# Performance work log

Hardware: AMD Instinct MI355X
Metric: run time of the kernel (lower is better)

## Reference

```python
import jax, jax.numpy as jnp
import numpy as np
from jax import lax

D_MODEL = 1024
D_INNER = 2048
B = 8
T = 2048
INIT_ALPHA_BIAS = 2.0


def setup_inputs() -> dict:
    key = jax.random.key(0)
    ks = jax.random.split(key, 6)
    def xavier(k, shape):
        fan_in, fan_out = shape[1], shape[0]
        lim = float(np.sqrt(6.0 / (fan_in + fan_out)))
        return jax.random.uniform(k, shape, jnp.float32, -lim, lim)
    return {
        "x": jax.random.normal(ks[0], (B, T, D_MODEL), jnp.float32),
        "h0": jnp.zeros((B, D_INNER), jnp.float32),
        "W_in": xavier(ks[1], (D_INNER, D_MODEL)),
        "W_alpha": xavier(ks[2], (D_INNER, D_INNER)),
        "b_alpha": jnp.full((D_INNER,), INIT_ALPHA_BIAS, jnp.float32),
        "W_v": xavier(ks[3], (D_INNER, D_INNER)),
        "b_v": jnp.zeros((D_INNER,), jnp.float32),
        "W_out": xavier(ks[4], (D_MODEL, D_INNER)),
    }


def reference(x, h0, W_in, W_alpha, b_alpha, W_v, b_v, W_out):
    # in_proj + silu pre-activation: [B,T,D_inner]
    x_proj = jax.nn.silu(jnp.einsum('btd,id->bti', x, W_in))
    # time-major for the scan: [T,B,D_inner]
    xr = jnp.transpose(x_proj, (1, 0, 2))
    # precompute gate and value for all steps (big GEMMs)
    alpha = jax.nn.sigmoid(jnp.einsum('tbd,ed->tbe', xr, W_alpha) + b_alpha)
    v = jnp.einsum('tbd,ed->tbe', xr, W_v) + b_v

    def step(h, av):
        a, vt = av
        h_new = a * h + (1.0 - a) * vt  # decay-gated update
        out_t = h_new * jax.nn.silu(h_new)  # self-gating
        return h_new, out_t

    h_final, outs = lax.scan(step, h0, (alpha, v))  # outs: [T,B,D_inner]
    # out_proj back to model dim, batch-major: [B,T,D_model]
    output = jnp.einsum('tbe,de->btd', outs, W_out)
    return output, h_final
```

## Files before the change

kernel.cpp:

```cpp
#include <hip/hip_runtime.h>
#include <cstdint>
#include <cstddef>

typedef unsigned short u16;
typedef unsigned int   u32;

#define D_MODEL 1024
#define D_INNER 2048
#define BATCH   8
#define TSEQ    2048
#define MROWS   (BATCH*TSEQ)
#define CHUNK   32
#define NCHUNK  (TSEQ/CHUNK)
#define EDIM    (BATCH*D_INNER)

typedef float  f32x4  __attribute__((ext_vector_type(4)));
typedef __bf16 bf16x8 __attribute__((ext_vector_type(8)));
typedef short  s16x8  __attribute__((ext_vector_type(8)));

__device__ __forceinline__ float bf2f(u16 u){ return __builtin_bit_cast(float, (u32)u << 16); }
__device__ __forceinline__ u16 f2bf(float f){
  u32 u = __builtin_bit_cast(u32, f);
  u += 0x7fffu + ((u >> 16) & 1u);
  return (u16)(u >> 16);
}
__device__ __forceinline__ float sigm(float x){ return 1.0f/(1.0f + __expf(-x)); }

__device__ __forceinline__ void gld16(const u16* g, u16* l){
  __builtin_amdgcn_global_load_lds((const __attribute__((address_space(1))) void*)g,
                                   (__attribute__((address_space(3))) void*)l, 16, 0, 0);
}

__device__ __forceinline__ s16x8 cvt8(const float* s){
  float4 u0 = *(const float4*)s;
  float4 u1 = *(const float4*)(s + 4);
  s16x8 p;
  p[0]=(short)f2bf(u0.x); p[1]=(short)f2bf(u0.y);
  p[2]=(short)f2bf(u0.z); p[3]=(short)f2bf(u0.w);
  p[4]=(short)f2bf(u1.x); p[5]=(short)f2bf(u1.y);
  p[6]=(short)f2bf(u1.z); p[7]=(short)f2bf(u1.w);
  return p;
}

template<int MODE, int K, int N>
__global__ __launch_bounds__(512, 2) void gemm256(
    const u16* __restrict__ A, const u16* __restrict__ Bt,
    const float* __restrict__ bias, const float* __restrict__ bias2,
    void* __restrict__ Cout, void* __restrict__ Cout2)
{
  __shared__ __align__(16) u16 sAB[2][2][16384];
  constexpr int NT = K/64;
  const int tid = threadIdx.x;
  const int w = tid >> 6, lane = tid & 63;
  const int wr = w >> 2, wc = w & 3;
  const int l15 = lane & 15, kg = lane >> 4;
  const int bm = blockIdx.x, bn = blockIdx.y;

  const int st_rw   = lane >> 3;
  const int st_cole = ((lane&7) ^ st_rw) << 3;
  const size_t a_base = (size_t)(bm*256)*K + st_cole;
  const size_t b_base = (size_t)(bn*256)*K + st_cole;

  auto stageA = [&](int buf, int kt, int set){
    u16* dst = &sAB[0][buf][set*4096 + w*512];
    #pragma unroll
    for (int i = 0; i < 2; ++i){
      const int row = set*64 + i*128 + w*8 + st_rw;
      gld16(A + a_base + (size_t)row*K + kt*64, dst + i*8192);
    }
  };
  auto stageB = [&](int buf, int kt, int set){
    #pragma unroll
    for (int i = 0; i < 2; ++i){
      const int g = i*64 + w*8;
      const int rowbase = (g>>5)*64 + set*32 + (g&31);
      gld16(Bt + b_base + (size_t)(rowbase + st_rw)*K + kt*64,
            &sAB[1][buf][rowbase*64]);
    }
  };

  const int csw = (kg*16) ^ ((l15&7)<<4);

  f32x4 acc[8][4] = {};

  stageB(0,0,0); stageB(0,0,1); stageA(0,0,0); stageA(0,0,1);

  for (int t = 0; t < NT; ++t){
    const char* As = (const char*)&sAB[0][t&1][0];
    const char* Bs = (const char*)&sAB[1][t&1][0];
    const int nb = (t+1)&1;

    asm volatile("s_waitcnt vmcnt(0)" ::: "memory");
    __builtin_amdgcn_s_barrier();

    if (t < NT-1){
      stageB(nb,t+1,0); stageB(nb,t+1,1); stageA(nb,t+1,0); stageA(nb,t+1,1);
    }

    s16x8 bf[4][2];
    #pragma unroll
    for (int ni = 0; ni < 4; ++ni){
      bf[ni][0] = *(const s16x8*)(Bs + (wc*64 + ni*16 + l15)*128 + csw);
      bf[ni][1] = *(const s16x8*)(Bs + (wc*64 + ni*16 + l15)*128 + (csw^64));
    }
    #pragma unroll
    for (int mh = 0; mh < 2; ++mh){
      s16x8 af[4][2];
      #pragma unroll
      for (int mf = 0; mf < 4; ++mf){
        af[mf][0] = *(const s16x8*)(As + (wr*128 + mh*64 + mf*16 + l15)*128 + csw);
        af[mf][1] = *(const s16x8*)(As + (wr*128 + mh*64 + mf*16 + l15)*128 + (csw^64));
      }
      #pragma unroll
      for (int mf = 0; mf < 4; ++mf)
        #pragma unroll
        for (int ni = 0; ni < 4; ++ni)
          #pragma unroll
          for (int ks = 0; ks < 2; ++ks)
            acc[mh*4+mf][ni] = __builtin_amdgcn_mfma_f32_16x16x32_bf16(
                __builtin_bit_cast(bf16x8, af[mf][ks]),
                __builtin_bit_cast(bf16x8, bf[ni][ks]),
                acc[mh*4+mf][ni], 0, 0, 0);
    }
  }

  #pragma unroll
  for (int mi = 0; mi < 8; ++mi){
    #pragma unroll
    for (int ni = 0; ni < 4; ++ni){
      #pragma unroll
      for (int r = 0; r < 4; ++r){
        const int row = bm*256 + wr*128 + mi*16 + kg*4 + r;
        const int col = bn*256 + wc*64 + ni*16 + l15;
        float val = acc[mi][ni][r];
        if constexpr (MODE == 0){
          val = val * sigm(val);
          ((u16*)Cout)[(size_t)row*N + col] = f2bf(val);
        } else if constexpr (MODE == 3){
          const int orow = (row & 7)*TSEQ + (row >> 3);
          ((float*)Cout)[(size_t)orow*N + col] = val;
        } else if constexpr (MODE == 4){
          if (col < D_INNER){
            val = sigm(val + bias[col]);
            ((u16*)Cout)[(size_t)row*D_INNER + col] = f2bf(val);
          } else {
            val = val + bias2[col - D_INNER];
            ((u16*)Cout2)[(size_t)row*D_INNER + (col - D_INNER)] = f2bf(val);
          }
        }
      }
    }
  }
}

template<int MODE, int K, int N, bool BA, bool BB>
__global__ __launch_bounds__(256) void gemm_bt(
    const void* __restrict__ Ap, const void* __restrict__ Bp,
    const float* __restrict__ bias, void* __restrict__ Cout)
{
  __shared__ __align__(16) u16 sA[128*32];
  __shared__ __align__(16) u16 sB[128*32];
  const int tid = threadIdx.x;
  const int bm = blockIdx.x, bn = blockIdx.y;
  const int w = tid >> 6, lane = tid & 63;
  const int wr = w >> 1, wc = w & 1;
  const int l15 = lane & 15, kg = lane >> 4;
  const int r0   = tid >> 2;
  const int koff = (tid & 3) * 8;

  int ga[2];
  #pragma unroll
  for (int i = 0; i < 2; ++i){
    int mc = bm*128 + r0 + i*64;
    if (MODE == 0)      ga[i] = (mc & 7) * TSEQ + (mc >> 3);
    else if (MODE == 3) ga[i] = (mc & (TSEQ-1)) * BATCH + (mc >> 11);
    else                ga[i] = mc;
  }
  const u16*   Abf = (const u16*)Ap;
  const float* Af  = (const float*)Ap;
  const u16*   Bbf = (const u16*)Bp;
  const float* Bf  = (const float*)Bp;
  u16* la[2] = { sA + w*512, sA + 2048 + w*512 };
  u16* lb[2] = { sB + w*512, sB + 2048 + w*512 };
  u16* ldsA = sA + tid*8;
  u16* ldsB = sB + tid*8;
  const int gb[2] = { bn*128 + r0, bn*128 + r0 + 64 };

  f32x4 acc[4][4] = {};
  for (int kt = 0; kt < K/32; ++kt){
    __syncthreads();
    if constexpr (BA){
      gld16(Abf + (size_t)ga[0]*K + koff + kt*32, la[0]);
      gld16(Abf + (size_t)ga[1]*K + koff + kt*32, la[1]);
    } else {
      #pragma unroll
      for (int i = 0; i < 2; ++i)
        *(s16x8*)(ldsA + i*2048) = cvt8(Af + (size_t)ga[i]*K + koff + kt*32);
    }
    if constexpr (BB){
      gld16(Bbf + (size_t)gb[0]*K + koff + kt*32, lb[0]);
      gld16(Bbf + (size_t)gb[1]*K + koff + kt*32, lb[1]);
    } else {
      #pragma unroll
      for (int i = 0; i < 2; ++i)
        *(s16x8*)(ldsB + i*2048) = cvt8(Bf + (size_t)gb[i]*K + koff + kt*32);
    }
    __syncthreads();

    s16x8 af[4], bfr[4];
    #pragma unroll
    for (int m = 0; m < 4; ++m)
      af[m] = *(const s16x8*)(sA + (wr*64 + m*16 + l15)*32 + kg*8);
    #pragma unroll
    for (int n = 0; n < 4; ++n)
      bfr[n] = *(const s16x8*)(sB + (wc*64 + n*16 + l15)*32 + kg*8);
    #pragma unroll
    for (int m = 0; m < 4; ++m)
      #pragma unroll
      for (int n = 0; n < 4; ++n)
        acc[m][n] = __builtin_amdgcn_mfma_f32_16x16x32_bf16(
            __builtin_bit_cast(bf16x8, af[m]),
            __builtin_bit_cast(bf16x8, bfr[n]),
            acc[m][n], 0, 0, 0);
  }
  #pragma unroll
  for (int m = 0; m < 4; ++m)
    #pragma unroll
    for (int n = 0; n < 4; ++n)
      #pragma unroll
      for (int r = 0; r < 4; ++r){
        const int row = bm*128 + wr*64 + m*16 + kg*4 + r;
        const int col = bn*128 + wc*64 + n*16 + l15;
        float val = acc[m][n][r];
        if constexpr (MODE == 0){
          val = val * sigm(val);
          ((u16*)Cout)[(size_t)row*N + col] = f2bf(val);
        } else if constexpr (MODE == 1){
          val = sigm(val + bias[col]);
          ((u16*)Cout)[(size_t)row*N + col] = f2bf(val);
        } else if constexpr (MODE == 2){
          val = val + bias[col];
          ((u16*)Cout)[(size_t)row*N + col] = f2bf(val);
        } else {
          ((float*)Cout)[(size_t)row*N + col] = val;
        }
      }
}

__global__ __launch_bounds__(256) void scan_pass1(
    const u16* __restrict__ alpha, const u16* __restrict__ v,
    float* __restrict__ P, float* __restrict__ H)
{
  const int e = blockIdx.x*256 + threadIdx.x;
  const int c = blockIdx.y;
  const size_t base = (size_t)c*CHUNK*EDIM + e;
  float p = 1.f, h = 0.f;
  #pragma unroll 8
  for (int t = 0; t < CHUNK; ++t){
    float a  = bf2f(alpha[base + (size_t)t*EDIM]);
    float vv = bf2f(v[base + (size_t)t*EDIM]);
    p *= a;
    h = a*h + (1.f - a)*vv;
  }
  P[(size_t)c*EDIM + e] = p;
  H[(size_t)c*EDIM + e] = h;
}

__global__ __launch_bounds__(256) void scan_pass2(
    const float* __restrict__ P, const float* __restrict__ H,
    const float* __restrict__ h0, float* __restrict__ hstart,
    float* __restrict__ hfinal)
{
  const int e = blockIdx.x*256 + threadIdx.x;
  float hs = h0[e];
  for (int c = 0; c < NCHUNK; ++c){
    hstart[(size_t)c*EDIM + e] = hs;
    hs = P[(size_t)c*EDIM + e]*hs + H[(size_t)c*EDIM + e];
  }
  hfinal[e] = hs;
}

__global__ __launch_bounds__(256) void scan_pass3(
    const u16* __restrict__ alpha, const u16* __restrict__ v,
    const float* __restrict__ hstart, u16* __restrict__ outs)
{
  const int e = blockIdx.x*256 + threadIdx.x;
  const int c = blockIdx.y;
  const size_t base = (size_t)c*CHUNK*EDIM + e;
  float h = hstart[(size_t)c*EDIM + e];
  #pragma unroll 8
  for (int t = 0; t < CHUNK; ++t){
    float a  = bf2f(alpha[base + (size_t)t*EDIM]);
    float vv = bf2f(v[base + (size_t)t*EDIM]);
    h = a*h + (1.f - a)*vv;
    float o = h*h*sigm(h);
    outs[base + (size_t)t*EDIM] = f2bf(o);
  }
}

__global__ __launch_bounds__(256) void cvt_bf16(
    const float* __restrict__ src, u16* __restrict__ dst, int n4)
{
  const int i = blockIdx.x*256 + threadIdx.x;
  if (i >= n4) return;
  const float4 f = ((const float4*)src)[i];
  u32 w0 = (u32)f2bf(f.x) | ((u32)f2bf(f.y) << 16);
  u32 w1 = (u32)f2bf(f.z) | ((u32)f2bf(f.w) << 16);
  ((uint2*)dst)[i] = make_uint2(w0, w1);
}

__global__ __launch_bounds__(256) void cvt_x_tm(
    const float* __restrict__ src, u16* __restrict__ dst)
{
  const int i = blockIdx.x*256 + threadIdx.x;
  const int d4  = i & 255;
  const int rin = i >> 8;
  const int b = rin >> 11, tt = rin & (TSEQ-1);
  const int rout = tt*BATCH + b;
  const float4 f = ((const float4*)src)[i];
  u32 w0 = (u32)f2bf(f.x) | ((u32)f2bf(f.y) << 16);
  u32 w1 = (u32)f2bf(f.z) | ((u32)f2bf(f.w) << 16);
  ((uint2*)dst)[(size_t)rout*256 + d4] = make_uint2(w0, w1);
}

extern "C" void kernel_launch(void* const* d_in, const int* in_sizes, int n_in,
                              void* d_out, int out_size, void* d_ws, size_t ws_size,
                              hipStream_t stream)
{
  const float* x     = (const float*)d_in[0];
  const float* h0    = (const float*)d_in[1];
  const float* W_in  = (const float*)d_in[2];
  const float* W_al  = (const float*)d_in[3];
  const float* b_al  = (const float*)d_in[4];
  const float* W_v   = (const float*)d_in[5];
  const float* b_v   = (const float*)d_in[6];
  const float* W_out = (const float*)d_in[7];

  float* out  = (float*)d_out;
  float* hfin = out + (size_t)MROWS*D_MODEL;

  const size_t SZ_ACT = (size_t)MROWS*D_INNER*2;
  const size_t SZ_ST  = (size_t)NCHUNK*EDIM*4;
  const size_t SZ_WI  = (size_t)D_INNER*D_MODEL*2;
  const size_t SZ_WA  = (size_t)D_INNER*D_INNER*2;
  const size_t need_min  = 3*SZ_ACT + 3*SZ_ST;
  const size_t need_fast = need_min + 2*SZ_WI + 2*SZ_WA + 8192;

  if (ws_size < need_min) return;

  char* ws = (char*)d_ws;
  auto carve = [&](size_t bytes){
    char* p = ws; ws += (bytes + 255) & ~(size_t)255; return p;
  };
  u16* xp   = (u16*)carve(SZ_ACT);
  u16* alp  = (u16*)carve(SZ_ACT);
  u16* vv   = (u16*)carve(SZ_ACT);
  float* P  = (float*)carve(SZ_ST);
  float* H  = (float*)carve(SZ_ST);
  float* hs = (float*)carve(SZ_ST);

  const dim3 gScan(EDIM/256, NCHUNK);

  auto cvt = [&](const float* s, u16* d, size_t n){
    int n4 = (int)(n/4);
    cvt_bf16<<<(n4+255)/256, 256, 0, stream>>>(s, d, n4);
  };

  if (ws_size >= need_fast){
    u16* wib = (u16*)carve(SZ_WI);
    u16* wab = (u16*)carve(SZ_WA);
    u16* wvb = (u16*)carve(SZ_WA);
    u16* wob = (u16*)carve(SZ_WI);
    u16* xb  = alp;

    cvt_x_tm<<<(MROWS*D_MODEL/4)/256, 256, 0, stream>>>(x, xb);
    cvt(W_in,  wib, (size_t)D_INNER*D_MODEL);
    cvt(W_al,  wab, (size_t)D_INNER*D_INNER);
    cvt(W_v,   wvb, (size_t)D_INNER*D_INNER);
    cvt(W_out, wob, (size_t)D_MODEL*D_INNER);

    gemm256<0, D_MODEL, D_INNER><<<dim3(MROWS/256, D_INNER/256), 512, 0, stream>>>(
        xb, wib, nullptr, nullptr, xp, nullptr);
    gemm256<4, D_INNER, 2*D_INNER><<<dim3(MROWS/256, 2*D_INNER/256), 512, 0, stream>>>(
        xp, wab, b_al, b_v, alp, vv);

    scan_pass1<<<gScan, 256, 0, stream>>>(alp, vv, P, H);
    scan_pass2<<<EDIM/256, 256, 0, stream>>>(P, H, h0, hs, hfin);
    scan_pass3<<<gScan, 256, 0, stream>>>(alp, vv, hs, vv);

    gemm256<3, D_INNER, D_MODEL><<<dim3(MROWS/256, D_MODEL/256), 512, 0, stream>>>(
        vv, wob, nullptr, nullptr, out, nullptr);
  } else {
    const dim3 gBig(MROWS/128, D_INNER/128);
    const dim3 gOut(MROWS/128, D_MODEL/128);
    gemm_bt<0, D_MODEL, D_INNER, false, false><<<gBig, 256, 0, stream>>>(x,  W_in, nullptr, xp);
    gemm_bt<1, D_INNER, D_INNER, true,  false><<<gBig, 256, 0, stream>>>(xp, W_al, b_al,    alp);
    gemm_bt<2, D_INNER, D_INNER, true,  false><<<gBig, 256, 0, stream>>>(xp, W_v,  b_v,     vv);

    scan_pass1<<<gScan, 256, 0, stream>>>(alp, vv, P, H);
    scan_pass2<<<EDIM/256, 256, 0, stream>>>(P, H, h0, hs, hfin);
    scan_pass3<<<gScan, 256, 0, stream>>>(alp, vv, hs, vv);

    gemm_bt<3, D_INNER, D_MODEL, true, false><<<gOut, 256, 0, stream>>>(vv, W_out, nullptr, out);
  }
}
```

Measured before the change: 539.7 us.

## Interleave GEMM global-to-LDS staging with MFMA quadrants using fine-grained waits

Restructures the GEMM main loop into four quadrant phases. Each phase reads an A/B fragment half from LDS, issues one quarter of the next tile's global-to-LDS loads, then waits with partial vmcnt and barriers before running its MFMA block under raised priority. This replaces a single full vmcnt(0) wait plus barrier per K-tile, so memory latency can overlap compute. The last iteration is peeled to drain the loads. Cost: many more barriers, and correctness relies on the vmcnt counts matching the load-issue order exactly.

New measurement: 547.9 us. Within noise of the previous version (+1.5%).

```diff
diff --git a/kernel.cpp b/kernel.cpp
--- a/kernel.cpp
+++ b/kernel.cpp
@@ -42,6 +42,36 @@
   return p;
 }
 
+#define RD_A(MH) \
+  _Pragma("unroll") \
+  for (int mf = 0; mf < 4; ++mf){ \
+    af[mf][0] = *(const s16x8*)(As + (wr*128 + (MH)*64 + mf*16 + l15)*128 + csw); \
+    af[mf][1] = *(const s16x8*)(As + (wr*128 + (MH)*64 + mf*16 + l15)*128 + (csw^64)); \
+  }
+#define RD_B(NH) \
+  _Pragma("unroll") \
+  for (int nf = 0; nf < 2; ++nf){ \
+    bf[nf][0] = *(const s16x8*)(Bs + (wc*64 + (NH)*32 + nf*16 + l15)*128 + csw); \
+    bf[nf][1] = *(const s16x8*)(Bs + (wc*64 + (NH)*32 + nf*16 + l15)*128 + (csw^64)); \
+  }
+#define MF(MH, NH) \
+  __builtin_amdgcn_s_setprio(1); \
+  _Pragma("unroll") \
+  for (int mf = 0; mf < 4; ++mf) \
+    _Pragma("unroll") \
+    for (int nf = 0; nf < 2; ++nf) \
+      _Pragma("unroll") \
+      for (int ks = 0; ks < 2; ++ks) \
+        acc[(MH)*4+mf][(NH)*2+nf] = __builtin_amdgcn_mfma_f32_16x16x32_bf16( \
+            __builtin_bit_cast(bf16x8, af[mf][ks]), \
+            __builtin_bit_cast(bf16x8, bf[nf][ks]), \
+            acc[(MH)*4+mf][(NH)*2+nf], 0, 0, 0); \
+  __builtin_amdgcn_s_setprio(0);
+
+#define SBAR()  __builtin_amdgcn_sched_barrier(0)
+#define BAR()   __builtin_amdgcn_s_barrier()
+#define VM(N)   asm volatile("s_waitcnt vmcnt(" #N ")" ::: "memory")
+
 template<int MODE, int K, int N>
 __global__ __launch_bounds__(512, 2) void gemm256(
     const u16* __restrict__ A, const u16* __restrict__ Bt,
@@ -82,46 +112,65 @@
   const int csw = (kg*16) ^ ((l15&7)<<4);
 
   f32x4 acc[8][4] = {};
-
-  stageB(0,0,0); stageB(0,0,1); stageA(0,0,0); stageA(0,0,1);
-
-  for (int t = 0; t < NT; ++t){
+  s16x8 af[4][2], bf[2][2];
+
+  stageB(0,0,0); stageA(0,0,0); stageB(0,0,1); stageA(0,0,1);
+  VM(4);
+  BAR();
+
+  for (int t = 0; t < NT-1; ++t){
     const char* As = (const char*)&sAB[0][t&1][0];
     const char* Bs = (const char*)&sAB[1][t&1][0];
     const int nb = (t+1)&1;
 
-    asm volatile("s_waitcnt vmcnt(0)" ::: "memory");
-    __builtin_amdgcn_s_barrier();
-
-    if (t < NT-1){
-      stageB(nb,t+1,0); stageB(nb,t+1,1); stageA(nb,t+1,0); stageA(nb,t+1,1);
-    }
-
-    s16x8 bf[4][2];
-    #pragma unroll
-    for (int ni = 0; ni < 4; ++ni){
-      bf[ni][0] = *(const s16x8*)(Bs + (wc*64 + ni*16 + l15)*128 + csw);
-      bf[ni][1] = *(const s16x8*)(Bs + (wc*64 + ni*16 + l15)*128 + (csw^64));
-    }
-    #pragma unroll
-    for (int mh = 0; mh < 2; ++mh){
-      s16x8 af[4][2];
-      #pragma unroll
-      for (int mf = 0; mf < 4; ++mf){
-        af[mf][0] = *(const s16x8*)(As + (wr*128 + mh*64 + mf*16 + l15)*128 + csw);
-        af[mf][1] = *(const s16x8*)(As + (wr*128 + mh*64 + mf*16 + l15)*128 + (csw^64));
-      }
-      #pragma unroll
-      for (int mf = 0; mf < 4; ++mf)
-        #pragma unroll
-        for (int ni = 0; ni < 4; ++ni)
-          #pragma unroll
-          for (int ks = 0; ks < 2; ++ks)
-            acc[mh*4+mf][ni] = __builtin_amdgcn_mfma_f32_16x16x32_bf16(
-                __builtin_bit_cast(bf16x8, af[mf][ks]),
-                __builtin_bit_cast(bf16x8, bf[ni][ks]),
-                acc[mh*4+mf][ni], 0, 0, 0);
-    }
+    RD_A(0) RD_B(0)
+    stageB(nb,t+1,0);
+    SBAR(); VM(4); BAR(); SBAR();
+    MF(0,0)
+    SBAR(); BAR();
+
+    RD_B(1)
+    stageA(nb,t+1,0);
+    SBAR(); VM(4); BAR(); SBAR();
+    MF(0,1)
+    SBAR(); BAR();
+
+    RD_A(1)
+    stageB(nb,t+1,1);
+    SBAR(); BAR(); SBAR();
+    MF(1,1)
+    SBAR(); BAR();
+
+    RD_B(0)
+    stageA(nb,t+1,1);
+    SBAR(); VM(4); BAR(); SBAR();
+    MF(1,0)
+    SBAR(); BAR();
+  }
+
+  {
+    const int t = NT-1;
+    const char* As = (const char*)&sAB[0][t&1][0];
+    const char* Bs = (const char*)&sAB[1][t&1][0];
+
+    RD_A(0) RD_B(0)
+    SBAR(); VM(2); BAR(); SBAR();
+    MF(0,0)
+    SBAR(); BAR();
+
+    RD_B(1)
+    SBAR(); VM(0); BAR(); SBAR();
+    MF(0,1)
+    SBAR(); BAR();
+
+    RD_A(1)
+    SBAR(); BAR(); SBAR();
+    MF(1,1)
+    SBAR(); BAR();
+
+    RD_B(0)
+    SBAR(); BAR(); SBAR();
+    MF(1,0)
   }
 
   #pragma unroll
```

## Load B fragments directly from global into registers, skipping LDS staging

Applied to the files above, without the earlier changes.

The GEMM kernel no longer stages the B tile through shared memory. Each wave loads its B fragments straight from global memory into registers after the MFMA loop of the current step, and only A is double-buffered in LDS. This halves LDS use and removes the LDS reads for B, which could allow higher occupancy. In exchange, B reuse across the two warp-rows is lost, so global and L2 traffic for B doubles. The register-held B loads are also exposed to the vmcnt(0) wait at the top of the next iteration.

New measurement: 815.8 us. 51.2% more time.

```diff
diff --git a/kernel.cpp b/kernel.cpp
--- a/kernel.cpp
+++ b/kernel.cpp
@@ -48,7 +48,7 @@
     const float* __restrict__ bias, const float* __restrict__ bias2,
     void* __restrict__ Cout, void* __restrict__ Cout2)
 {
-  __shared__ __align__(16) u16 sAB[2][2][16384];
+  __shared__ __align__(16) u16 sA[2][16384];
   constexpr int NT = K/64;
   const int tid = threadIdx.x;
   const int w = tid >> 6, lane = tid & 63;
@@ -59,50 +59,42 @@
   const int st_rw   = lane >> 3;
   const int st_cole = ((lane&7) ^ st_rw) << 3;
   const size_t a_base = (size_t)(bm*256)*K + st_cole;
-  const size_t b_base = (size_t)(bn*256)*K + st_cole;
 
   auto stageA = [&](int buf, int kt, int set){
-    u16* dst = &sAB[0][buf][set*4096 + w*512];
+    u16* dst = &sA[buf][set*4096 + w*512];
     #pragma unroll
     for (int i = 0; i < 2; ++i){
       const int row = set*64 + i*128 + w*8 + st_rw;
       gld16(A + a_base + (size_t)row*K + kt*64, dst + i*8192);
     }
   };
-  auto stageB = [&](int buf, int kt, int set){
-    #pragma unroll
-    for (int i = 0; i < 2; ++i){
-      const int g = i*64 + w*8;
-      const int rowbase = (g>>5)*64 + set*32 + (g&31);
-      gld16(Bt + b_base + (size_t)(rowbase + st_rw)*K + kt*64,
-            &sAB[1][buf][rowbase*64]);
-    }
+
+  const u16* bptr = Bt + (size_t)(bn*256 + wc*64 + l15)*K + kg*8;
+  s16x8 bf[4][2];
+  auto loadB = [&](int kt){
+    #pragma unroll
+    for (int ni = 0; ni < 4; ++ni)
+      #pragma unroll
+      for (int ks = 0; ks < 2; ++ks)
+        bf[ni][ks] = *(const s16x8*)(bptr + (size_t)ni*16*K + kt*64 + ks*32);
   };
 
   const int csw = (kg*16) ^ ((l15&7)<<4);
 
   f32x4 acc[8][4] = {};
 
-  stageB(0,0,0); stageB(0,0,1); stageA(0,0,0); stageA(0,0,1);
+  stageA(0,0,0); stageA(0,0,1);
+  loadB(0);
 
   for (int t = 0; t < NT; ++t){
-    const char* As = (const char*)&sAB[0][t&1][0];
-    const char* Bs = (const char*)&sAB[1][t&1][0];
+    const char* As = (const char*)&sA[t&1][0];
     const int nb = (t+1)&1;
 
     asm volatile("s_waitcnt vmcnt(0)" ::: "memory");
     __builtin_amdgcn_s_barrier();
 
-    if (t < NT-1){
-      stageB(nb,t+1,0); stageB(nb,t+1,1); stageA(nb,t+1,0); stageA(nb,t+1,1);
-    }
-
-    s16x8 bf[4][2];
-    #pragma unroll
-    for (int ni = 0; ni < 4; ++ni){
-      bf[ni][0] = *(const s16x8*)(Bs + (wc*64 + ni*16 + l15)*128 + csw);
-      bf[ni][1] = *(const s16x8*)(Bs + (wc*64 + ni*16 + l15)*128 + (csw^64));
-    }
+    if (t < NT-1){ stageA(nb,t+1,0); stageA(nb,t+1,1); }
+
     #pragma unroll
     for (int mh = 0; mh < 2; ++mh){
       s16x8 af[4][2];
@@ -122,6 +114,9 @@
                 __builtin_bit_cast(bf16x8, bf[ni][ks]),
                 acc[mh*4+mf][ni], 0, 0, 0);
     }
+
+    __builtin_amdgcn_sched_barrier(0);
+    if (t < NT-1) loadB(t+1);
   }
 
   #pragma unroll
```
